# Kernel optimization log

Measured on AMD Instinct MI355X. Metric: run time of the kernel, lower is better.

Reference implementation:

```python
import jax, jax.numpy as jnp
import numpy as np

N_NODES = 100000
N_EDGES = 1600000
IN_FEATS = 256
OUT_FEATS = 128


def setup_inputs() -> dict:
    key = jax.random.key(0)
    k1, k2, k3, k4, k5 = jax.random.split(key, 5)
    x = jax.random.normal(k1, (N_NODES, IN_FEATS), dtype=jnp.float32)
    edge_row = jax.random.randint(k2, (N_EDGES,), 0, N_NODES, dtype=jnp.int64 if jax.config.jax_enable_x64 else jnp.int32)
    edge_col = jax.random.randint(k3, (N_EDGES,), 0, N_NODES, dtype=jnp.int64 if jax.config.jax_enable_x64 else jnp.int32)
    edge_val = jax.random.uniform(k4, (N_EDGES,), dtype=jnp.float32)
    # xavier_uniform-like init for weight
    limit = float(np.sqrt(6.0 / (IN_FEATS + OUT_FEATS)))
    weight = jax.random.uniform(k5, (IN_FEATS, OUT_FEATS), dtype=jnp.float32, minval=-limit, maxval=limit)
    b = jnp.zeros((OUT_FEATS,), dtype=jnp.float32)
    return {"x": x, "edge_row": edge_row, "edge_col": edge_col, "edge_val": edge_val, "weight": weight, "b": b}


def reference(x, edge_row, edge_col, edge_val, weight, b):
    # sup = input @ weight : [N, out_feats]
    sup = x @ weight
    # out = spmm(adj, sup): gather source rows, scale by edge value, scatter-add to dest
    msgs = edge_val[:, None] * sup[edge_col]          # [E, out_feats]
    out = jax.ops.segment_sum(msgs, edge_row, num_segments=N_NODES)  # [N, out_feats]
    return out + b
```

## Files before the change

### kernel.cpp

```cpp
#include <hip/hip_runtime.h>


#define K_FEATS 256
#define N_FEATS 128
#define BSHIFT 7
#define BROWS 128
#define BCAP 3072
#define CHUNK 8192
#define EPT 32

typedef __attribute__((ext_vector_type(8))) short short8;
typedef __attribute__((ext_vector_type(4))) float float4v;

__device__ __forceinline__ unsigned short f2bf(float f) {
    unsigned int u = __float_as_uint(f);
    unsigned int r = u + 0x7FFF + ((u >> 16) & 1);
    return (unsigned short)(r >> 16);
}

__global__ __launch_bounds__(256) void prep_w(const float* __restrict__ w,
                                              unsigned short* __restrict__ wt) {
    int n = blockIdx.x;
    int k = threadIdx.x;
    wt[n * K_FEATS + k] = f2bf(w[k * N_FEATS + n]);
}

__global__ __launch_bounds__(256) void gcn_gemm_mfma(const float* __restrict__ x,
                                                     const unsigned short* __restrict__ wt,
                                                     unsigned short* __restrict__ sup, int M) {
    __shared__ __align__(16) unsigned short As[128 * 40];

    const int tid  = threadIdx.x;
    const int wv   = tid >> 6;
    const int lane = tid & 63;
    const int l15  = lane & 15;
    const int quad = lane >> 4;
    const int row0 = blockIdx.x * 128;

    float4v acc[2][8];
#pragma unroll
    for (int mt = 0; mt < 2; mt++)
#pragma unroll
        for (int nt = 0; nt < 8; nt++) acc[mt][nt] = (float4v)(0.f);

    for (int k0 = 0; k0 < K_FEATS; k0 += 32) {
#pragma unroll
        for (int l = 0; l < 4; l++) {
            int f   = tid + l * 256;
            int r   = f >> 3;
            int k4  = f & 7;
            int grow = row0 + r;
            float4 v = make_float4(0.f, 0.f, 0.f, 0.f);
            if (grow < M) v = *(const float4*)(x + (long)grow * K_FEATS + k0 + k4 * 4);
            unsigned int p0 = (unsigned int)f2bf(v.x) | ((unsigned int)f2bf(v.y) << 16);
            unsigned int p1 = (unsigned int)f2bf(v.z) | ((unsigned int)f2bf(v.w) << 16);
            *(uint2*)(&As[r * 40 + k4 * 4]) = make_uint2(p0, p1);
        }
        __syncthreads();

        short8 afrag[2];
#pragma unroll
        for (int mt = 0; mt < 2; mt++) {
            afrag[mt] = *(const short8*)(&As[(wv * 32 + mt * 16 + l15) * 40 + quad * 8]);
        }
        short8 bfrag[8];
#pragma unroll
        for (int nt = 0; nt < 8; nt++) {
            bfrag[nt] = *(const short8*)(wt + (nt * 16 + l15) * K_FEATS + k0 + quad * 8);
        }
#pragma unroll
        for (int mt = 0; mt < 2; mt++)
#pragma unroll
            for (int nt = 0; nt < 8; nt++)
                acc[mt][nt] = __builtin_amdgcn_mfma_f32_16x16x32_bf16(
                    afrag[mt], bfrag[nt], acc[mt][nt], 0, 0, 0);
        __syncthreads();
    }

#pragma unroll
    for (int mt = 0; mt < 2; mt++) {
#pragma unroll
        for (int reg = 0; reg < 4; reg++) {
            int grow = row0 + wv * 32 + mt * 16 + quad * 4 + reg;
            if (grow < M) {
#pragma unroll
                for (int nt = 0; nt < 8; nt++) {
                    sup[(long)grow * N_FEATS + nt * 16 + l15] = f2bf(acc[mt][nt][reg]);
                }
            }
        }
    }
}

__global__ __launch_bounds__(256) void zero_ints(int* __restrict__ p, int n) {
    int i = blockIdx.x * 256 + threadIdx.x;
    if (i < n) p[i] = 0;
}

__global__ __launch_bounds__(256) void wg_partition(const int* __restrict__ erow,
                                                    const int* __restrict__ ecol,
                                                    const float* __restrict__ eval_,
                                                    int* __restrict__ bcur,
                                                    int2* __restrict__ tmp, int E, int NB) {
    __shared__ int hist[1024];
    __shared__ int cur[1024];
    const int tid = threadIdx.x;
    const long e0 = (long)blockIdx.x * CHUNK;

    for (int i = tid; i < NB; i += 256) hist[i] = 0;
    __syncthreads();

    int rows[EPT];
#pragma unroll
    for (int i = 0; i < EPT; i++) {
        long e = e0 + tid + i * 256;
        int r = -1;
        if (e < E) {
            r = erow[e];
            atomicAdd(&hist[r >> BSHIFT], 1);
        }
        rows[i] = r;
    }
    __syncthreads();

    for (int i = tid; i < NB; i += 256) {
        int c = hist[i];
        cur[i] = c ? atomicAdd(&bcur[i], c) : 0;
    }
    __syncthreads();

#pragma unroll
    for (int i = 0; i < EPT; i++) {
        long e = e0 + tid + i * 256;
        if (e >= E) continue;
        int r = rows[i];
        int b = r >> BSHIFT;
        int p = atomicAdd(&cur[b], 1);
        if (p < BCAP)
            tmp[(long)b * BCAP + p] = make_int2(((r & (BROWS - 1)) << 17) | ecol[e],
                                                __float_as_int(eval_[e]));
    }
}

__global__ __launch_bounds__(1024) void bucket_scan(const int* __restrict__ bcnt,
                                                    int* __restrict__ bbase,
                                                    int* __restrict__ off0,
                                                    int NB, int M) {
    __shared__ int sm[1024];
    int t = threadIdx.x;
    int v = 0;
    if (t < NB) { v = bcnt[t]; if (v > BCAP) v = BCAP; }
    sm[t] = v;
    __syncthreads();
#pragma unroll
    for (int s = 1; s < 1024; s <<= 1) {
        int a = (t >= s) ? sm[t - s] : 0;
        __syncthreads();
        sm[t] += a;
        __syncthreads();
    }
    if (t < NB) bbase[t] = sm[t] - v;
    if (t == 1023) off0[M] = sm[1023];
}

__global__ __launch_bounds__(256) void bucket_to_sorted(const int* __restrict__ bcnt,
                                                        const int* __restrict__ bbase,
                                                        const int2* __restrict__ tmp,
                                                        int* __restrict__ off0,
                                                        int2* __restrict__ sedge, int M) {
    __shared__ int hist[BROWS];
    __shared__ int cur[BROWS];
    const int b   = blockIdx.x;
    const int tid = threadIdx.x;
    const int row0 = b << BSHIFT;

    if (tid < BROWS) hist[tid] = 0;
    __syncthreads();

    int cnt = bcnt[b];
    if (cnt > BCAP) cnt = BCAP;
    const int2* t = tmp + (long)b * BCAP;

    for (int i = tid; i < cnt; i += 256)
        atomicAdd(&hist[(unsigned)t[i].x >> 17], 1);
    __syncthreads();

    if (tid < BROWS) cur[tid] = hist[tid];
    __syncthreads();
#pragma unroll
    for (int s = 1; s < BROWS; s <<= 1) {
        int v = 0;
        if (tid >= s && tid < BROWS) v = cur[tid - s];
        __syncthreads();
        if (tid < BROWS) cur[tid] += v;
        __syncthreads();
    }

    const int base = bbase[b];
    if (tid < BROWS) {
        int start = base + cur[tid] - hist[tid];
        cur[tid] = start;
        if (row0 + tid < M) off0[row0 + tid] = start;
    }
    __syncthreads();

    for (int i = tid; i < cnt; i += 256) {
        int2 e = t[i];
        int rl = (unsigned)e.x >> 17;
        int p = atomicAdd(&cur[rl], 1);
        sedge[p] = make_int2(e.x & 0x1FFFF, e.y);
    }
}

__global__ __launch_bounds__(256) void gcn_spmm(const int* __restrict__ off0,
                                                const int2* __restrict__ sedge,
                                                const unsigned short* __restrict__ sup,
                                                const float* __restrict__ b,
                                                float* __restrict__ out, int M) {
    int row  = blockIdx.x * 4 + (threadIdx.x >> 6);
    if (row >= M) return;
    int lane = threadIdx.x & 63;
    int half = lane >> 5;
    int l31  = lane & 31;
    int s = off0[row], e = off0[row + 1];
    const uint2* sup64 = (const uint2*)sup;

    float4v acc = (float4v)(0.f);
    int base = s;
    for (; base + 8 <= e; base += 8) {
        int2 ed[4];
#pragma unroll
        for (int u = 0; u < 4; u++) ed[u] = sedge[base + half + 2 * u];
        uint2 g[4];
#pragma unroll
        for (int u = 0; u < 4; u++) g[u] = sup64[(long)ed[u].x * 32 + l31];
#pragma unroll
        for (int u = 0; u < 4; u++) {
            float v = __int_as_float(ed[u].y);
            acc.x += v * __uint_as_float(g[u].x << 16);
            acc.y += v * __uint_as_float(g[u].x & 0xFFFF0000u);
            acc.z += v * __uint_as_float(g[u].y << 16);
            acc.w += v * __uint_as_float(g[u].y & 0xFFFF0000u);
        }
    }
    for (int i = base + half; i < e; i += 2) {
        int2 ed = sedge[i];
        uint2 g = sup64[(long)ed.x * 32 + l31];
        float v = __int_as_float(ed.y);
        acc.x += v * __uint_as_float(g.x << 16);
        acc.y += v * __uint_as_float(g.x & 0xFFFF0000u);
        acc.z += v * __uint_as_float(g.y << 16);
        acc.w += v * __uint_as_float(g.y & 0xFFFF0000u);
    }

    acc.x += __shfl_xor(acc.x, 32);
    acc.y += __shfl_xor(acc.y, 32);
    acc.z += __shfl_xor(acc.z, 32);
    acc.w += __shfl_xor(acc.w, 32);

    if (half == 0) {
        float4v bb = ((const float4v*)b)[l31];
        acc += bb;
        *(float4v*)(out + (long)row * N_FEATS + l31 * 4) = acc;
    }
}

extern "C" void kernel_launch(void* const* d_in, const int* in_sizes, int n_in,
                              void* d_out, int out_size, void* d_ws, size_t ws_size,
                              hipStream_t stream) {
    const float* x     = (const float*)d_in[0];
    const int*   erow  = (const int*)d_in[1];
    const int*   ecol  = (const int*)d_in[2];
    const float* eval_ = (const float*)d_in[3];
    const float* w     = (const float*)d_in[4];
    const float* b     = (const float*)d_in[5];
    float* out = (float*)d_out;

    const int M  = in_sizes[0] / K_FEATS;
    const int E  = in_sizes[1];
    const int NB = (M + BROWS - 1) >> BSHIFT;

    size_t o_sup   = 0;
    size_t o_wt    = o_sup   + (((size_t)M * N_FEATS * 2 + 15) & ~15ul);
    size_t o_off0  = o_wt    + (size_t)K_FEATS * N_FEATS * 2;
    size_t o_bcur  = o_off0  + (((size_t)(M + 1) * 4 + 15) & ~15ul);
    size_t o_bbase = o_bcur  + (((size_t)NB * 4 + 15) & ~15ul);
    size_t o_tmp   = o_bbase + (((size_t)NB * 4 + 15) & ~15ul);
    size_t o_edge  = o_tmp   + ((size_t)NB * BCAP * 8);

    unsigned short* sup   = (unsigned short*)((char*)d_ws + o_sup);
    unsigned short* wt    = (unsigned short*)((char*)d_ws + o_wt);
    int*            off0  = (int*)((char*)d_ws + o_off0);
    int*            bcur  = (int*)((char*)d_ws + o_bcur);
    int*            bbase = (int*)((char*)d_ws + o_bbase);
    int2*           tmp   = (int2*)((char*)d_ws + o_tmp);
    int2*           sedge = (int2*)((char*)d_ws + o_edge);

    prep_w<<<N_FEATS, 256, 0, stream>>>(w, wt);
    gcn_gemm_mfma<<<(M + 127) / 128, 256, 0, stream>>>(x, wt, sup, M);

    zero_ints<<<(NB + 255) / 256, 256, 0, stream>>>(bcur, NB);
    int nchunks = (E + CHUNK - 1) / CHUNK;
    wg_partition<<<nchunks, 256, 0, stream>>>(erow, ecol, eval_, bcur, tmp, E, NB);
    bucket_scan<<<1, 1024, 0, stream>>>(bcur, bbase, off0, NB, M);
    bucket_to_sorted<<<NB, 256, 0, stream>>>(bcur, bbase, tmp, off0, sedge, M);

    gcn_spmm<<<(M + 3) / 4, 256, 0, stream>>>(off0, sedge, sup, b, out, M);
}
```

Before: 358.5 us.

## Fuse GEMM and edge partition into one interleaved launch, drop LDS staging

The dense GEMM and the edge bucket-partition kernel are merged into one launch. Every fifth block runs a partition chunk and the remaining blocks run GEMM tiles, so the two independent memory-bound stages overlap on the GPU and one launch boundary disappears. The GEMM also stops staging A through shared memory: each wave loads its x rows straight from global memory into bf16 MFMA fragments, which removes the block barriers. The cost is a larger fused kernel whose register use is set by the heavier path, plus less cooperative load coalescing for x.

```diff
diff --git a/kernel.cpp b/kernel.cpp
--- a/kernel.cpp
+++ b/kernel.cpp
@@ -8,6 +8,7 @@
 #define BCAP 3072
 #define CHUNK 8192
 #define EPT 32
+#define RMOD 5
 
 typedef __attribute__((ext_vector_type(8))) short short8;
 typedef __attribute__((ext_vector_type(4))) float float4v;
@@ -25,17 +26,71 @@
     wt[n * K_FEATS + k] = f2bf(w[k * N_FEATS + n]);
 }
 
-__global__ __launch_bounds__(256) void gcn_gemm_mfma(const float* __restrict__ x,
-                                                     const unsigned short* __restrict__ wt,
-                                                     unsigned short* __restrict__ sup, int M) {
-    __shared__ __align__(16) unsigned short As[128 * 40];
-
-    const int tid  = threadIdx.x;
+__global__ __launch_bounds__(256) void zero_ints(int* __restrict__ p, int n) {
+    int i = blockIdx.x * 256 + threadIdx.x;
+    if (i < n) p[i] = 0;
+}
+
+__global__ __launch_bounds__(256) void gemm_partition(
+        const float* __restrict__ x, const unsigned short* __restrict__ wt,
+        unsigned short* __restrict__ sup, int M, int NT,
+        const int* __restrict__ erow, const int* __restrict__ ecol,
+        const float* __restrict__ eval_, int* __restrict__ bcur,
+        int2* __restrict__ tmp, int E, int NB, int NCH) {
+    __shared__ int hist[1024];
+    __shared__ int cur[1024];
+    const int g   = blockIdx.x;
+    const int tid = threadIdx.x;
+
+    if (g % RMOD == 0) {
+        int pid = g / RMOD;
+        if (pid >= NCH) return;
+        const long e0 = (long)pid * CHUNK;
+
+        for (int i = tid; i < NB; i += 256) hist[i] = 0;
+        __syncthreads();
+
+        int rows[EPT];
+#pragma unroll
+        for (int i = 0; i < EPT; i++) {
+            long e = e0 + tid + i * 256;
+            int r = -1;
+            if (e < E) {
+                r = erow[e];
+                atomicAdd(&hist[r >> BSHIFT], 1);
+            }
+            rows[i] = r;
+        }
+        __syncthreads();
+
+        for (int i = tid; i < NB; i += 256) {
+            int c = hist[i];
+            cur[i] = c ? atomicAdd(&bcur[i], c) : 0;
+        }
+        __syncthreads();
+
+#pragma unroll
+        for (int i = 0; i < EPT; i++) {
+            long e = e0 + tid + i * 256;
+            if (e >= E) continue;
+            int r = rows[i];
+            int b = r >> BSHIFT;
+            int p = atomicAdd(&cur[b], 1);
+            if (p < BCAP)
+                tmp[(long)b * BCAP + p] = make_int2(((r & (BROWS - 1)) << 17) | ecol[e],
+                                                    __float_as_int(eval_[e]));
+        }
+        return;
+    }
+
+    int tile = g - g / RMOD - 1;
+    if (tile >= NT) return;
+
     const int wv   = tid >> 6;
     const int lane = tid & 63;
     const int l15  = lane & 15;
     const int quad = lane >> 4;
-    const int row0 = blockIdx.x * 128;
+    const int row0 = tile * 128 + wv * 32;
 
     float4v acc[2][8];
 #pragma unroll
@@ -43,25 +98,25 @@
 #pragma unroll
         for (int nt = 0; nt < 8; nt++) acc[mt][nt] = (float4v)(0.f);
 
+#pragma unroll 2
     for (int k0 = 0; k0 < K_FEATS; k0 += 32) {
-#pragma unroll
-        for (int l = 0; l < 4; l++) {
-            int f   = tid + l * 256;
-            int r   = f >> 3;
-            int k4  = f & 7;
-            int grow = row0 + r;
-            float4 v = make_float4(0.f, 0.f, 0.f, 0.f);
-            if (grow < M) v = *(const float4*)(x + (long)grow * K_FEATS + k0 + k4 * 4);
-            unsigned int p0 = (unsigned int)f2bf(v.x) | ((unsigned int)f2bf(v.y) << 16);
-            unsigned int p1 = (unsigned int)f2bf(v.z) | ((unsigned int)f2bf(v.w) << 16);
-            *(uint2*)(&As[r * 40 + k4 * 4]) = make_uint2(p0, p1);
-        }
-        __syncthreads();
-
         short8 afrag[2];
 #pragma unroll
         for (int mt = 0; mt < 2; mt++) {
-            afrag[mt] = *(const short8*)(&As[(wv * 32 + mt * 16 + l15) * 40 + quad * 8]);
+            int grow = row0 + mt * 16 + l15;
+            float4 a0 = make_float4(0.f, 0.f, 0.f, 0.f);
+            float4 a1 = make_float4(0.f, 0.f, 0.f, 0.f);
+            if (grow < M) {
+                const float* p = x + (long)grow * K_FEATS + k0 + quad * 8;
+                a0 = *(const float4*)p;
+                a1 = *(const float4*)(p + 4);
+            }
+            short8 af;
+            af[0] = (short)f2bf(a0.x); af[1] = (short)f2bf(a0.y);
+            af[2] = (short)f2bf(a0.z); af[3] = (short)f2bf(a0.w);
+            af[4] = (short)f2bf(a1.x); af[5] = (short)f2bf(a1.y);
+            af[6] = (short)f2bf(a1.z); af[7] = (short)f2bf(a1.w);
+            afrag[mt] = af;
         }
         short8 bfrag[8];
 #pragma unroll
@@ -74,14 +129,13 @@
             for (int nt = 0; nt < 8; nt++)
                 acc[mt][nt] = __builtin_amdgcn_mfma_f32_16x16x32_bf16(
                     afrag[mt], bfrag[nt], acc[mt][nt], 0, 0, 0);
-        __syncthreads();
     }
 
 #pragma unroll
     for (int mt = 0; mt < 2; mt++) {
 #pragma unroll
         for (int reg = 0; reg < 4; reg++) {
-            int grow = row0 + wv * 32 + mt * 16 + quad * 4 + reg;
+            int grow = row0 + mt * 16 + quad * 4 + reg;
             if (grow < M) {
 #pragma unroll
                 for (int nt = 0; nt < 8; nt++) {
@@ -89,56 +143,6 @@
                 }
             }
         }
-    }
-}
-
-__global__ __launch_bounds__(256) void zero_ints(int* __restrict__ p, int n) {
-    int i = blockIdx.x * 256 + threadIdx.x;
-    if (i < n) p[i] = 0;
-}
-
-__global__ __launch_bounds__(256) void wg_partition(const int* __restrict__ erow,
-                                                    const int* __restrict__ ecol,
-                                                    const float* __restrict__ eval_,
-                                                    int* __restrict__ bcur,
-                                                    int2* __restrict__ tmp, int E, int NB) {
-    __shared__ int hist[1024];
-    __shared__ int cur[1024];
-    const int tid = threadIdx.x;
-    const long e0 = (long)blockIdx.x * CHUNK;
-
-    for (int i = tid; i < NB; i += 256) hist[i] = 0;
-    __syncthreads();
-
-    int rows[EPT];
-#pragma unroll
-    for (int i = 0; i < EPT; i++) {
-        long e = e0 + tid + i * 256;
-        int r = -1;
-        if (e < E) {
-            r = erow[e];
-            atomicAdd(&hist[r >> BSHIFT], 1);
-        }
-        rows[i] = r;
-    }
-    __syncthreads();
-
-    for (int i = tid; i < NB; i += 256) {
-        int c = hist[i];
-        cur[i] = c ? atomicAdd(&bcur[i], c) : 0;
-    }
-    __syncthreads();
-
-#pragma unroll
-    for (int i = 0; i < EPT; i++) {
-        long e = e0 + tid + i * 256;
-        if (e >= E) continue;
-        int r = rows[i];
-        int b = r >> BSHIFT;
-        int p = atomicAdd(&cur[b], 1);
-        if (p < BCAP)
-            tmp[(long)b * BCAP + p] = make_int2(((r & (BROWS - 1)) << 17) | ecol[e],
-                                                __float_as_int(eval_[e]));
     }
 }
 
@@ -279,6 +283,8 @@
     const int M  = in_sizes[0] / K_FEATS;
     const int E  = in_sizes[1];
     const int NB = (M + BROWS - 1) >> BSHIFT;
+    const int NT = (M + 127) / 128;
+    const int NCH = (E + CHUNK - 1) / CHUNK;
 
     size_t o_sup   = 0;
     size_t o_wt    = o_sup   + (((size_t)M * N_FEATS * 2 + 15) & ~15ul);
@@ -297,11 +303,12 @@
     int2*           sedge = (int2*)((char*)d_ws + o_edge);
 
     prep_w<<<N_FEATS, 256, 0, stream>>>(w, wt);
-    gcn_gemm_mfma<<<(M + 127) / 128, 256, 0, stream>>>(x, wt, sup, M);
-
     zero_ints<<<(NB + 255) / 256, 256, 0, stream>>>(bcur, NB);
-    int nchunks = (E + CHUNK - 1) / CHUNK;
-    wg_partition<<<nchunks, 256, 0, stream>>>(erow, ecol, eval_, bcur, tmp, E, NB);
+
+    int nblk = NT + NCH;
+    gemm_partition<<<nblk, 256, 0, stream>>>(x, wt, sup, M, NT,
+                                             erow, ecol, eval_, bcur, tmp, E, NB, NCH);
+
     bucket_scan<<<1, 1024, 0, stream>>>(bcur, bbase, off0, NB, M);
     bucket_to_sorted<<<NB, 256, 0, stream>>>(bcur, bbase, tmp, off0, sedge, M);
 
```

Result: faster. 329.3 us (-8.1%).
